# Kernel tuning notes

Measured on AMD Instinct MI355X. Metric: run time of the kernel, lower is better.

The kernel has to match this reference:

```python
import jax, jax.numpy as jnp
import numpy as np

ALPHA = 0.2  # LeakyReLU negative slope


def setup_inputs() -> dict:
    key = jax.random.key(0)
    k1, k2 = jax.random.split(key)
    B, N, Fin, Fout = 4, 4096, 256, 128
    h = jax.random.normal(k1, (B, N, Fin), dtype=jnp.float32)
    adj = jnp.zeros((B, N, N), dtype=bool)  # unused by the original forward
    # Linear(in,out,bias=False); stored as [in,out] for h @ W
    W = jax.random.normal(k2, (Fin, Fout), dtype=jnp.float32) * (1.0 / np.sqrt(Fin))
    return {"h": h, "adj": adj, "W": W}


def reference(h, adj, W):
    # h: [B,N,Fin], W: [Fin,Fout]
    hp = jnp.einsum("bnf,fo->bno", h, W)                    # [B,N,Fout]
    e = jnp.einsum("bnd,bmd->bnm", hp, hp)                  # [B,N,N]
    e = jnp.where(e >= 0, e, ALPHA * e)                      # LeakyReLU
    attn = jax.nn.softmax(e, axis=1)                         # softmax over dim=1 (rows)
    # torch: sum_j( hp[b,i] * attn[b,i,j] ) == hp[b,i] * sum_j attn[b,i,j]
    row_mass = jnp.sum(attn, axis=2, keepdims=True)          # [B,N,1]
    return hp * row_mass
```

## Files before the change

kernel.cpp:

```cpp
#include <hip/hip_runtime.h>
#include <hip/hip_bf16.h>

#define ALPHA 0.2f

constexpr int BN   = 4;
constexpr int NN   = 4096;
constexpr int FIN  = 256;
constexpr int FOUT = 128;
constexpr int NT   = 64;
constexpr int NPAIR = NT * (NT + 1) / 2;

typedef __attribute__((ext_vector_type(8))) short bf16x8;
typedef __attribute__((ext_vector_type(4))) float f32x4;

#define MFMA16(a, b, c) __builtin_amdgcn_mfma_f32_16x16x32_bf16((a), (b), (c), 0, 0, 0)

template<int CTRL>
__device__ __forceinline__ float dpp_mov(float x) {
    return __int_as_float(__builtin_amdgcn_update_dpp(
        __float_as_int(x), __float_as_int(x), CTRL, 0xF, 0xF, false));
}
__device__ __forceinline__ float rsum16(float x) {
    x += dpp_mov<0x128>(x);
    x += dpp_mov<0x124>(x);
    x += dpp_mov<0x122>(x);
    x += dpp_mov<0x121>(x);
    return x;
}
__device__ __forceinline__ float rmax16(float x) {
    x = fmaxf(x, dpp_mov<0x128>(x));
    x = fmaxf(x, dpp_mov<0x124>(x));
    x = fmaxf(x, dpp_mov<0x122>(x));
    x = fmaxf(x, dpp_mov<0x121>(x));
    return x;
}

__device__ __forceinline__ void split8(const float* x, uint4& H, uint4& L) {
    ushort hb[8], lb[8];
    #pragma unroll
    for (int i = 0; i < 8; ++i) {
        float xv = x[i];
        __hip_bfloat16 hh = __float2bfloat16(xv);
        float hf = __bfloat162float(hh);
        __hip_bfloat16 lw = __float2bfloat16(xv - hf);
        hb[i] = reinterpret_cast<const ushort&>(hh);
        lb[i] = reinterpret_cast<const ushort&>(lw);
    }
    H = make_uint4((uint)hb[0] | ((uint)hb[1] << 16), (uint)hb[2] | ((uint)hb[3] << 16),
                   (uint)hb[4] | ((uint)hb[5] << 16), (uint)hb[6] | ((uint)hb[7] << 16));
    L = make_uint4((uint)lb[0] | ((uint)lb[1] << 16), (uint)lb[2] | ((uint)lb[3] << 16),
                   (uint)lb[4] | ((uint)lb[5] << 16), (uint)lb[6] | ((uint)lb[7] << 16));
}

template<int ROWS, int KGSH>
__device__ __forceinline__ void stage_split(const float* __restrict__ src, int strideF,
                                            ushort* hi, ushort* lo, int tid) {
    constexpr int KG = 1 << KGSH;
    #pragma unroll
    for (int idx = tid; idx < ROWS * KG; idx += 256) {
        int row = idx >> KGSH, g = idx & (KG - 1);
        const float4* p4 = reinterpret_cast<const float4*>(src + (size_t)row * strideF + g * 8);
        float4 u = p4[0], v = p4[1];
        float x[8] = {u.x, u.y, u.z, u.w, v.x, v.y, v.z, v.w};
        uint4 H, L;
        split8(x, H, L);
        int gran = (row << KGSH) + (g ^ (row & 7));
        reinterpret_cast<uint4*>(hi)[gran] = H;
        reinterpret_cast<uint4*>(lo)[gran] = L;
    }
}
template<int ROWS, int KGSH>
__device__ __forceinline__ void stage_copy(const ushort* __restrict__ src, int strideU,
                                           ushort* dst, int tid) {
    constexpr int KG = 1 << KGSH;
    #pragma unroll
    for (int idx = tid; idx < ROWS * KG; idx += 256) {
        int row = idx >> KGSH, g = idx & (KG - 1);
        uint4 vv = *reinterpret_cast<const uint4*>(src + (size_t)row * strideU + g * 8);
        reinterpret_cast<uint4*>(dst)[(row << KGSH) + (g ^ (row & 7))] = vv;
    }
}
__device__ __forceinline__ bf16x8 frag16(const ushort* s, int rowbase, int kstep, int kgsh, int lane) {
    int r = rowbase + (lane & 15);
    int g = kstep * 4 + (lane >> 4);
    int gran = (r << kgsh) + (g ^ (r & 7));
    return *reinterpret_cast<const bf16x8*>(s + gran * 8);
}

__global__ void k_prepW(const float* __restrict__ W, ushort* __restrict__ Wt_hi,
                        ushort* __restrict__ Wt_lo) {
    int idx = blockIdx.x * 256 + threadIdx.x;
    if (idx >= FOUT * (FIN / 8)) return;
    int n = idx >> 5, g = idx & 31;
    float x[8];
    #pragma unroll
    for (int i = 0; i < 8; ++i) x[i] = W[(size_t)(g * 8 + i) * FOUT + n];
    uint4 H, L;
    split8(x, H, L);
    reinterpret_cast<uint4*>(Wt_hi)[n * 32 + g] = H;
    reinterpret_cast<uint4*>(Wt_lo)[n * 32 + g] = L;
}

__global__ __launch_bounds__(256)
void k_hp(const float* __restrict__ h, const ushort* __restrict__ Wt_hi,
          const ushort* __restrict__ Wt_lo, float* __restrict__ hp) {
    __shared__ __align__(16) ushort Ah[64 * 64], Al[64 * 64];
    __shared__ __align__(16) ushort Bh[128 * 64], Bl[128 * 64];
    const int tid = threadIdx.x, lane = tid & 63, wid = tid >> 6;
    const int wy = wid >> 1, wx = wid & 1;
    const int ibase = blockIdx.x * 64;
    f32x4 z = {0.f, 0.f, 0.f, 0.f};
    f32x4 acc[2][4] = {{z, z, z, z}, {z, z, z, z}};
    for (int kt = 0; kt < 4; ++kt) {
        __syncthreads();
        stage_split<64, 3>(h + (size_t)ibase * FIN + kt * 64, FIN, Ah, Al, tid);
        stage_copy<128, 3>(Wt_hi + kt * 64, FIN, Bh, tid);
        stage_copy<128, 3>(Wt_lo + kt * 64, FIN, Bl, tid);
        __syncthreads();
        #pragma unroll
        for (int pr = 0; pr < 3; ++pr) {
            const ushort* A = (pr == 2) ? Al : Ah;
            const ushort* B = (pr == 1) ? Bl : Bh;
            #pragma unroll
            for (int ks = 0; ks < 2; ++ks) {
                bf16x8 a0 = frag16(A, wy * 32, ks, 3, lane);
                bf16x8 a1 = frag16(A, wy * 32 + 16, ks, 3, lane);
                #pragma unroll
                for (int c = 0; c < 4; ++c) {
                    bf16x8 bb = frag16(B, wx * 64 + c * 16, ks, 3, lane);
                    acc[0][c] = MFMA16(a0, bb, acc[0][c]);
                    acc[1][c] = MFMA16(a1, bb, acc[1][c]);
                }
            }
        }
    }
    #pragma unroll
    for (int r = 0; r < 2; ++r)
        #pragma unroll
        for (int c = 0; c < 4; ++c)
            #pragma unroll
            for (int p = 0; p < 4; ++p) {
                int row = ibase + wy * 32 + r * 16 + (lane >> 4) * 4 + p;
                int col = wx * 64 + c * 16 + (lane & 15);
                hp[(size_t)row * FOUT + col] = acc[r][c][p];
            }
}

__global__ void k_fragpack(const float* __restrict__ hp, ushort* __restrict__ hi,
                           ushort* __restrict__ lo) {
    int t = blockIdx.x * 256 + threadIdx.x;
    int l = t & 63, ks = (t >> 6) & 3, P = (t >> 8) & 255, b = t >> 16;
    int row = P * 16 + (l & 15), c8 = ks * 4 + (l >> 4);
    const float* src = hp + ((size_t)b * NN + row) * FOUT + c8 * 8;
    const float4* p4 = reinterpret_cast<const float4*>(src);
    float4 u = p4[0], v = p4[1];
    float x[8] = {u.x, u.y, u.z, u.w, v.x, v.y, v.z, v.w};
    uint4 H, L;
    split8(x, H, L);
    size_t o = (((size_t)b * 256 + P) * 4 + ks) * 64 + l;
    reinterpret_cast<uint4*>(hi)[o] = H;
    reinterpret_cast<uint4*>(lo)[o] = L;
}

__device__ __forceinline__ void decode2(int bid, int wid, int& b, int& ti, int& tj) {
    int slot = bid & 7;
    b = slot >> 1;
    int sub = ((bid >> 3) << 1) | (slot & 1);
    int tb = sub * 4 + wid;
    int t = 0, width = NT;
    while (tb >= width) { tb -= width; --width; ++t; }
    ti = t;
    tj = t + tb;
}

__device__ __forceinline__ void etile_fl(const uint4* __restrict__ H4,
                                         const uint4* __restrict__ L4,
                                         int pi, int pj, int lane, f32x4 acc[4][4]) {
    #pragma unroll
    for (int ks = 0; ks < 4; ++ks) {
        bf16x8 aH[4], aL[4];
        #pragma unroll
        for (int r = 0; r < 4; ++r) {
            size_t idx = ((size_t)(pi + r) * 4 + ks) * 64 + lane;
            aH[r] = *reinterpret_cast<const bf16x8*>(&H4[idx]);
            aL[r] = *reinterpret_cast<const bf16x8*>(&L4[idx]);
        }
        #pragma unroll
        for (int c = 0; c < 4; ++c) {
            size_t jdx = ((size_t)(pj + c) * 4 + ks) * 64 + lane;
            bf16x8 bH = *reinterpret_cast<const bf16x8*>(&H4[jdx]);
            bf16x8 bL = *reinterpret_cast<const bf16x8*>(&L4[jdx]);
            #pragma unroll
            for (int r = 0; r < 4; ++r) {
                acc[r][c] = MFMA16(aH[r], bH, acc[r][c]);
                acc[r][c] = MFMA16(aH[r], bL, acc[r][c]);
                acc[r][c] = MFMA16(aL[r], bH, acc[r][c]);
            }
        }
    }
}

__global__ __launch_bounds__(256, 3)
void k_stats(const ushort* __restrict__ hp_hi, const ushort* __restrict__ hp_lo,
             float* __restrict__ m_part, float* __restrict__ s_part) {
    const int tid = threadIdx.x, lane = tid & 63, wid = tid >> 6;
    const int lrow = lane & 15, lg = lane >> 4;
    int b, ti, tj;
    decode2(blockIdx.x, wid, b, ti, tj);
    const uint4* H4 = reinterpret_cast<const uint4*>(hp_hi) + (size_t)b * 256 * 256;
    const uint4* L4 = reinterpret_cast<const uint4*>(hp_lo) + (size_t)b * 256 * 256;
    const int ibase = ti * 64, jbase = tj * 64;
    f32x4 z = {0.f, 0.f, 0.f, 0.f};
    f32x4 acc[4][4] = {{z,z,z,z},{z,z,z,z},{z,z,z,z},{z,z,z,z}};
    etile_fl(H4, L4, ti * 4, tj * 4, lane, acc);
    #pragma unroll
    for (int r = 0; r < 4; ++r)
        #pragma unroll
        for (int c = 0; c < 4; ++c)
            #pragma unroll
            for (int p = 0; p < 4; ++p) {
                float x = acc[r][c][p];
                acc[r][c][p] = fmaxf(x, ALPHA * x);
            }
    {
        float* mp = m_part + (size_t)(b * NT + tj) * NN;
        float* sp = s_part + (size_t)(b * NT + tj) * NN;
        #pragma unroll
        for (int r = 0; r < 4; ++r)
            #pragma unroll
            for (int p = 0; p < 4; ++p) {
                float mx = fmaxf(fmaxf(acc[r][0][p], acc[r][1][p]),
                                 fmaxf(acc[r][2][p], acc[r][3][p]));
                mx = rmax16(mx);
                float se = 0.f;
                #pragma unroll
                for (int c = 0; c < 4; ++c) se += __expf(acc[r][c][p] - mx);
                se = rsum16(se);
                if (lrow == 0) {
                    int i = ibase + r * 16 + lg * 4 + p;
                    mp[i] = mx;
                    sp[i] = se;
                }
            }
    }
    if (ti != tj) {
        float* mp = m_part + (size_t)(b * NT + ti) * NN;
        float* sp = s_part + (size_t)(b * NT + ti) * NN;
        #pragma unroll
        for (int c = 0; c < 4; ++c) {
            float mx = -1e30f;
            #pragma unroll
            for (int r = 0; r < 4; ++r)
                #pragma unroll
                for (int p = 0; p < 4; ++p) mx = fmaxf(mx, acc[r][c][p]);
            mx = fmaxf(mx, __shfl_xor(mx, 16));
            mx = fmaxf(mx, __shfl_xor(mx, 32));
            float se = 0.f;
            #pragma unroll
            for (int r = 0; r < 4; ++r)
                #pragma unroll
                for (int p = 0; p < 4; ++p) se += __expf(acc[r][c][p] - mx);
            se += __shfl_xor(se, 16);
            se += __shfl_xor(se, 32);
            if (lane < 16) {
                int j = jbase + c * 16 + lane;
                mp[j] = mx;
                sp[j] = se;
            }
        }
    }
}

__global__ void k_merge(const float* __restrict__ m_part, const float* __restrict__ s_part,
                        float* __restrict__ m_fin, float* __restrict__ inv_s) {
    int idx = blockIdx.x * 256 + threadIdx.x;
    if (idx >= BN * NN) return;
    int b = idx >> 12, row = idx & (NN - 1);
    const float* mp = m_part + (size_t)b * NT * NN + row;
    const float* sp = s_part + (size_t)b * NT * NN + row;
    float M = -1e30f;
    for (int k = 0; k < NT; ++k) M = fmaxf(M, mp[(size_t)k * NN]);
    float S = 0.f;
    for (int k = 0; k < NT; ++k) S += sp[(size_t)k * NN] * __expf(mp[(size_t)k * NN] - M);
    m_fin[idx] = M;
    inv_s[idx] = 1.f / S;
}

__global__ __launch_bounds__(256, 3)
void k_mass(const ushort* __restrict__ hp_hi, const ushort* __restrict__ hp_lo,
            const float* __restrict__ m_fin, const float* __restrict__ inv_s,
            float* __restrict__ rs_part) {
    const int tid = threadIdx.x, lane = tid & 63, wid = tid >> 6;
    const int lrow = lane & 15, lg = lane >> 4;
    int b, ti, tj;
    decode2(blockIdx.x, wid, b, ti, tj);
    const uint4* H4 = reinterpret_cast<const uint4*>(hp_hi) + (size_t)b * 256 * 256;
    const uint4* L4 = reinterpret_cast<const uint4*>(hp_lo) + (size_t)b * 256 * 256;
    const int ibase = ti * 64, jbase = tj * 64;
    f32x4 z = {0.f, 0.f, 0.f, 0.f};
    f32x4 acc[4][4] = {{z,z,z,z},{z,z,z,z},{z,z,z,z},{z,z,z,z}};
    etile_fl(H4, L4, ti * 4, tj * 4, lane, acc);
    const float* mf = m_fin + (size_t)b * NN;
    const float* isv = inv_s + (size_t)b * NN;
    float mj[4], sj[4];
    #pragma unroll
    for (int c = 0; c < 4; ++c) {
        int j = jbase + c * 16 + lrow;
        mj[c] = mf[j];
        sj[c] = isv[j];
    }
    {
        float* rs = rs_part + (size_t)(b * NT + tj) * NN;
        #pragma unroll
        for (int r = 0; r < 4; ++r)
            #pragma unroll
            for (int p = 0; p < 4; ++p) {
                float s = 0.f;
                #pragma unroll
                for (int c = 0; c < 4; ++c) {
                    float x = acc[r][c][p];
                    float g = fmaxf(x, ALPHA * x);
                    s += __expf(g - mj[c]) * sj[c];
                }
                s = rsum16(s);
                if (lrow == 0) rs[ibase + r * 16 + lg * 4 + p] = s;
            }
    }
    if (ti != tj) {
        float mi[4][4], si_[4][4];
        #pragma unroll
        for (int r = 0; r < 4; ++r)
            #pragma unroll
            for (int p = 0; p < 4; ++p) {
                int i = ibase + r * 16 + lg * 4 + p;
                mi[r][p] = mf[i];
                si_[r][p] = isv[i];
            }
        float* rs = rs_part + (size_t)(b * NT + ti) * NN;
        #pragma unroll
        for (int c = 0; c < 4; ++c) {
            float s2 = 0.f;
            #pragma unroll
            for (int r = 0; r < 4; ++r)
                #pragma unroll
                for (int p = 0; p < 4; ++p) {
                    float x = acc[r][c][p];
                    float g = fmaxf(x, ALPHA * x);
                    s2 += __expf(g - mi[r][p]) * si_[r][p];
                }
            s2 += __shfl_xor(s2, 16);
            s2 += __shfl_xor(s2, 32);
            if (lane < 16) rs[jbase + c * 16 + lane] = s2;
        }
    }
}

__global__ void k_scale(const float* __restrict__ rs_part, float* __restrict__ out) {
    int idx = blockIdx.x * 256 + threadIdx.x;
    if (idx >= BN * NN * FOUT / 4) return;
    int row = idx >> 5;
    int b = row >> 12, i = row & (NN - 1);
    const float* rs = rs_part + (size_t)b * NT * NN + i;
    float rm = 0.f;
    for (int k = 0; k < NT; ++k) rm += rs[(size_t)k * NN];
    float4 v = reinterpret_cast<float4*>(out)[idx];
    v.x *= rm; v.y *= rm; v.z *= rm; v.w *= rm;
    reinterpret_cast<float4*>(out)[idx] = v;
}

extern "C" void kernel_launch(void* const* d_in, const int* in_sizes, int n_in,
                              void* d_out, int out_size, void* d_ws, size_t ws_size,
                              hipStream_t stream) {
    (void)in_sizes; (void)n_in; (void)out_size; (void)ws_size;
    const float* h = (const float*)d_in[0];
    const float* W = (const float*)d_in[2];
    float* out = (float*)d_out;
    ushort* hp_hi = (ushort*)d_ws;
    ushort* hp_lo = hp_hi + (size_t)BN * NN * FOUT;
    ushort* Wt_hi = hp_lo + (size_t)BN * NN * FOUT;
    ushort* Wt_lo = Wt_hi + FOUT * FIN;
    float* m_part = (float*)(Wt_lo + FOUT * FIN);
    float* s_part = m_part + (size_t)BN * NT * NN;
    float* m_fin  = s_part + (size_t)BN * NT * NN;
    float* inv_s  = m_fin + (size_t)BN * NN;
    float* rs_part = inv_s + (size_t)BN * NN;

    k_prepW<<<(FOUT * (FIN / 8) + 255) / 256, 256, 0, stream>>>(W, Wt_hi, Wt_lo);
    k_hp<<<BN * NN / 64, 256, 0, stream>>>(h, Wt_hi, Wt_lo, out);
    k_fragpack<<<BN * 256 * 4 * 64 / 256, 256, 0, stream>>>(out, hp_hi, hp_lo);
    k_stats<<<BN * NPAIR / 4, 256, 0, stream>>>(hp_hi, hp_lo, m_part, s_part);
    k_merge<<<(BN * NN + 255) / 256, 256, 0, stream>>>(m_part, s_part, m_fin, inv_s);
    k_mass<<<BN * NPAIR / 4, 256, 0, stream>>>(hp_hi, hp_lo, m_fin, inv_s, rs_part);
    k_scale<<<(BN * NN * FOUT / 4 + 255) / 256, 256, 0, stream>>>(rs_part, out);
}
```

Baseline: 418.6 us.

## Switch Gram tiles to 32x32x16 MFMA with repacked fragment layout

Replaces the 16x16x32 bf16 MFMA tiling of each 64x64 Gram tile with a 2x2 grid of 32x32x16 MFMAs, and repacks the hi/lo bf16 fragments in k_fragpack to match the 32-row operand layout. Row and column reductions in k_stats and k_mass are rewritten for the new accumulator lane mapping. Wave priority is raised around the MFMA loop. The goal is fewer operand loads per FLOP and higher MFMA throughput, at the cost of different reduction shuffles and per-element m/s loads in the column pass of k_mass.

```diff
diff --git a/kernel.cpp b/kernel.cpp
--- a/kernel.cpp
+++ b/kernel.cpp
@@ -12,8 +12,10 @@
 
 typedef __attribute__((ext_vector_type(8))) short bf16x8;
 typedef __attribute__((ext_vector_type(4))) float f32x4;
+typedef __attribute__((ext_vector_type(16))) float f32x16;
 
 #define MFMA16(a, b, c) __builtin_amdgcn_mfma_f32_16x16x32_bf16((a), (b), (c), 0, 0, 0)
+#define MFMA32(a, b, c) __builtin_amdgcn_mfma_f32_32x32x16_bf16((a), (b), (c), 0, 0, 0)
 
 template<int CTRL>
 __device__ __forceinline__ float dpp_mov(float x) {
@@ -149,17 +151,16 @@
 __global__ void k_fragpack(const float* __restrict__ hp, ushort* __restrict__ hi,
                            ushort* __restrict__ lo) {
     int t = blockIdx.x * 256 + threadIdx.x;
-    int l = t & 63, ks = (t >> 6) & 3, P = (t >> 8) & 255, b = t >> 16;
-    int row = P * 16 + (l & 15), c8 = ks * 4 + (l >> 4);
+    int l = t & 63, s = (t >> 6) & 7, Q = (t >> 9) & 127, b = t >> 16;
+    int row = Q * 32 + (l & 31), c8 = s * 2 + (l >> 5);
     const float* src = hp + ((size_t)b * NN + row) * FOUT + c8 * 8;
     const float4* p4 = reinterpret_cast<const float4*>(src);
     float4 u = p4[0], v = p4[1];
     float x[8] = {u.x, u.y, u.z, u.w, v.x, v.y, v.z, v.w};
     uint4 H, L;
     split8(x, H, L);
-    size_t o = (((size_t)b * 256 + P) * 4 + ks) * 64 + l;
-    reinterpret_cast<uint4*>(hi)[o] = H;
-    reinterpret_cast<uint4*>(lo)[o] = L;
+    reinterpret_cast<uint4*>(hi)[t] = H;
+    reinterpret_cast<uint4*>(lo)[t] = L;
 }
 
 __device__ __forceinline__ void decode2(int bid, int wid, int& b, int& ti, int& tj) {
@@ -173,71 +174,78 @@
     tj = t + tb;
 }
 
-__device__ __forceinline__ void etile_fl(const uint4* __restrict__ H4,
-                                         const uint4* __restrict__ L4,
-                                         int pi, int pj, int lane, f32x4 acc[4][4]) {
-    #pragma unroll
-    for (int ks = 0; ks < 4; ++ks) {
-        bf16x8 aH[4], aL[4];
-        #pragma unroll
-        for (int r = 0; r < 4; ++r) {
-            size_t idx = ((size_t)(pi + r) * 4 + ks) * 64 + lane;
-            aH[r] = *reinterpret_cast<const bf16x8*>(&H4[idx]);
-            aL[r] = *reinterpret_cast<const bf16x8*>(&L4[idx]);
-        }
-        #pragma unroll
-        for (int c = 0; c < 4; ++c) {
-            size_t jdx = ((size_t)(pj + c) * 4 + ks) * 64 + lane;
-            bf16x8 bH = *reinterpret_cast<const bf16x8*>(&H4[jdx]);
-            bf16x8 bL = *reinterpret_cast<const bf16x8*>(&L4[jdx]);
-            #pragma unroll
-            for (int r = 0; r < 4; ++r) {
-                acc[r][c] = MFMA16(aH[r], bH, acc[r][c]);
-                acc[r][c] = MFMA16(aH[r], bL, acc[r][c]);
-                acc[r][c] = MFMA16(aL[r], bH, acc[r][c]);
-            }
-        }
-    }
+__device__ __forceinline__ void etile32(const uint4* __restrict__ H4,
+                                        const uint4* __restrict__ L4,
+                                        int ti, int tj, int lane, f32x16 acc[2][2]) {
+    __builtin_amdgcn_s_setprio(1);
+    #pragma unroll
+    for (int s = 0; s < 8; ++s) {
+        bf16x8 aH[2], aL[2], bH[2], bL[2];
+        #pragma unroll
+        for (int R = 0; R < 2; ++R) {
+            size_t idx = ((size_t)((ti * 2 + R) * 8 + s)) * 64 + lane;
+            aH[R] = *reinterpret_cast<const bf16x8*>(&H4[idx]);
+            aL[R] = *reinterpret_cast<const bf16x8*>(&L4[idx]);
+        }
+        #pragma unroll
+        for (int C = 0; C < 2; ++C) {
+            size_t jdx = ((size_t)((tj * 2 + C) * 8 + s)) * 64 + lane;
+            bH[C] = *reinterpret_cast<const bf16x8*>(&H4[jdx]);
+            bL[C] = *reinterpret_cast<const bf16x8*>(&L4[jdx]);
+        }
+        #pragma unroll
+        for (int R = 0; R < 2; ++R)
+            #pragma unroll
+            for (int C = 0; C < 2; ++C) {
+                acc[R][C] = MFMA32(aH[R], bH[C], acc[R][C]);
+                acc[R][C] = MFMA32(aH[R], bL[C], acc[R][C]);
+                acc[R][C] = MFMA32(aL[R], bH[C], acc[R][C]);
+            }
+    }
+    __builtin_amdgcn_s_setprio(0);
 }
 
 __global__ __launch_bounds__(256, 3)
 void k_stats(const ushort* __restrict__ hp_hi, const ushort* __restrict__ hp_lo,
              float* __restrict__ m_part, float* __restrict__ s_part) {
     const int tid = threadIdx.x, lane = tid & 63, wid = tid >> 6;
-    const int lrow = lane & 15, lg = lane >> 4;
     int b, ti, tj;
     decode2(blockIdx.x, wid, b, ti, tj);
-    const uint4* H4 = reinterpret_cast<const uint4*>(hp_hi) + (size_t)b * 256 * 256;
-    const uint4* L4 = reinterpret_cast<const uint4*>(hp_lo) + (size_t)b * 256 * 256;
+    const uint4* H4 = reinterpret_cast<const uint4*>(hp_hi) + (size_t)b * 65536;
+    const uint4* L4 = reinterpret_cast<const uint4*>(hp_lo) + (size_t)b * 65536;
     const int ibase = ti * 64, jbase = tj * 64;
-    f32x4 z = {0.f, 0.f, 0.f, 0.f};
-    f32x4 acc[4][4] = {{z,z,z,z},{z,z,z,z},{z,z,z,z},{z,z,z,z}};
-    etile_fl(H4, L4, ti * 4, tj * 4, lane, acc);
-    #pragma unroll
-    for (int r = 0; r < 4; ++r)
-        #pragma unroll
-        for (int c = 0; c < 4; ++c)
-            #pragma unroll
-            for (int p = 0; p < 4; ++p) {
-                float x = acc[r][c][p];
-                acc[r][c][p] = fmaxf(x, ALPHA * x);
+    f32x16 acc[2][2];
+    #pragma unroll
+    for (int R = 0; R < 2; ++R)
+        #pragma unroll
+        for (int C = 0; C < 2; ++C)
+            #pragma unroll
+            for (int q = 0; q < 16; ++q) acc[R][C][q] = 0.f;
+    etile32(H4, L4, ti, tj, lane, acc);
+    #pragma unroll
+    for (int R = 0; R < 2; ++R)
+        #pragma unroll
+        for (int C = 0; C < 2; ++C)
+            #pragma unroll
+            for (int q = 0; q < 16; ++q) {
+                float x = acc[R][C][q];
+                acc[R][C][q] = fmaxf(x, ALPHA * x);
             }
     {
         float* mp = m_part + (size_t)(b * NT + tj) * NN;
         float* sp = s_part + (size_t)(b * NT + tj) * NN;
         #pragma unroll
-        for (int r = 0; r < 4; ++r)
-            #pragma unroll
-            for (int p = 0; p < 4; ++p) {
-                float mx = fmaxf(fmaxf(acc[r][0][p], acc[r][1][p]),
-                                 fmaxf(acc[r][2][p], acc[r][3][p]));
+        for (int R = 0; R < 2; ++R)
+            #pragma unroll
+            for (int q = 0; q < 16; ++q) {
+                float mx = fmaxf(acc[R][0][q], acc[R][1][q]);
                 mx = rmax16(mx);
-                float se = 0.f;
-                #pragma unroll
-                for (int c = 0; c < 4; ++c) se += __expf(acc[r][c][p] - mx);
+                mx = fmaxf(mx, __shfl_xor(mx, 16));
+                float se = __expf(acc[R][0][q] - mx) + __expf(acc[R][1][q] - mx);
                 se = rsum16(se);
-                if (lrow == 0) {
-                    int i = ibase + r * 16 + lg * 4 + p;
+                se += __shfl_xor(se, 16);
+                if ((lane & 31) == 0) {
+                    int i = ibase + R * 32 + (q & 3) + 8 * (q >> 2) + 4 * (lane >> 5);
                     mp[i] = mx;
                     sp[i] = se;
                 }
@@ -247,23 +255,21 @@
         float* mp = m_part + (size_t)(b * NT + ti) * NN;
         float* sp = s_part + (size_t)(b * NT + ti) * NN;
         #pragma unroll
-        for (int c = 0; c < 4; ++c) {
+        for (int C = 0; C < 2; ++C) {
             float mx = -1e30f;
             #pragma unroll
-            for (int r = 0; r < 4; ++r)
+            for (int R = 0; R < 2; ++R)
                 #pragma unroll
-                for (int p = 0; p < 4; ++p) mx = fmaxf(mx, acc[r][c][p]);
-            mx = fmaxf(mx, __shfl_xor(mx, 16));
+                for (int q = 0; q < 16; ++q) mx = fmaxf(mx, acc[R][C][q]);
             mx = fmaxf(mx, __shfl_xor(mx, 32));
             float se = 0.f;
             #pragma unroll
-            for (int r = 0; r < 4; ++r)
+            for (int R = 0; R < 2; ++R)
                 #pragma unroll
-                for (int p = 0; p < 4; ++p) se += __expf(acc[r][c][p] - mx);
-            se += __shfl_xor(se, 16);
+                for (int q = 0; q < 16; ++q) se += __expf(acc[R][C][q] - mx);
             se += __shfl_xor(se, 32);
-            if (lane < 16) {
-                int j = jbase + c * 16 + lane;
+            if (lane < 32) {
+                int j = jbase + C * 32 + lane;
                 mp[j] = mx;
                 sp[j] = se;
             }
@@ -291,66 +297,62 @@
             const float* __restrict__ m_fin, const float* __restrict__ inv_s,
             float* __restrict__ rs_part) {
     const int tid = threadIdx.x, lane = tid & 63, wid = tid >> 6;
-    const int lrow = lane & 15, lg = lane >> 4;
     int b, ti, tj;
     decode2(blockIdx.x, wid, b, ti, tj);
-    const uint4* H4 = reinterpret_cast<const uint4*>(hp_hi) + (size_t)b * 256 * 256;
-    const uint4* L4 = reinterpret_cast<const uint4*>(hp_lo) + (size_t)b * 256 * 256;
+    const uint4* H4 = reinterpret_cast<const uint4*>(hp_hi) + (size_t)b * 65536;
+    const uint4* L4 = reinterpret_cast<const uint4*>(hp_lo) + (size_t)b * 65536;
     const int ibase = ti * 64, jbase = tj * 64;
-    f32x4 z = {0.f, 0.f, 0.f, 0.f};
-    f32x4 acc[4][4] = {{z,z,z,z},{z,z,z,z},{z,z,z,z},{z,z,z,z}};
-    etile_fl(H4, L4, ti * 4, tj * 4, lane, acc);
+    f32x16 acc[2][2];
+    #pragma unroll
+    for (int R = 0; R < 2; ++R)
+        #pragma unroll
+        for (int C = 0; C < 2; ++C)
+            #pragma unroll
+            for (int q = 0; q < 16; ++q) acc[R][C][q] = 0.f;
+    etile32(H4, L4, ti, tj, lane, acc);
     const float* mf = m_fin + (size_t)b * NN;
     const float* isv = inv_s + (size_t)b * NN;
-    float mj[4], sj[4];
-    #pragma unroll
-    for (int c = 0; c < 4; ++c) {
-        int j = jbase + c * 16 + lrow;
-        mj[c] = mf[j];
-        sj[c] = isv[j];
+    float mj[2], sj[2];
+    #pragma unroll
+    for (int C = 0; C < 2; ++C) {
+        int j = jbase + C * 32 + (lane & 31);
+        mj[C] = mf[j];
+        sj[C] = isv[j];
     }
     {
         float* rs = rs_part + (size_t)(b * NT + tj) * NN;
         #pragma unroll
-        for (int r = 0; r < 4; ++r)
-            #pragma unroll
-            for (int p = 0; p < 4; ++p) {
-                float s = 0.f;
-                #pragma unroll
-                for (int c = 0; c < 4; ++c) {
-                    float x = acc[r][c][p];
-                    float g = fmaxf(x, ALPHA * x);
-                    s += __expf(g - mj[c]) * sj[c];
-                }
+        for (int R = 0; R < 2; ++R)
+            #pragma unroll
+            for (int q = 0; q < 16; ++q) {
+                float x0 = acc[R][0][q], x1 = acc[R][1][q];
+                float g0 = fmaxf(x0, ALPHA * x0), g1 = fmaxf(x1, ALPHA * x1);
+                float s = __expf(g0 - mj[0]) * sj[0] + __expf(g1 - mj[1]) * sj[1];
                 s = rsum16(s);
-                if (lrow == 0) rs[ibase + r * 16 + lg * 4 + p] = s;
+                s += __shfl_xor(s, 16);
+                if ((lane & 31) == 0)
+                    rs[ibase + R * 32 + (q & 3) + 8 * (q >> 2) + 4 * (lane >> 5)] = s;
             }
     }
     if (ti != tj) {
-        float mi[4][4], si_[4][4];
-        #pragma unroll
-        for (int r = 0; r < 4; ++r)
-            #pragma unroll
-            for (int p = 0; p < 4; ++p) {
-                int i = ibase + r * 16 + lg * 4 + p;
-                mi[r][p] = mf[i];
-                si_[r][p] = isv[i];
+        float s2[2] = {0.f, 0.f};
+        #pragma unroll
+        for (int R = 0; R < 2; ++R)
+            #pragma unroll
+            for (int q = 0; q < 16; ++q) {
+                int i = ibase + R * 32 + (q & 3) + 8 * (q >> 2) + 4 * (lane >> 5);
+                float m_i = mf[i];
+                float s_i = isv[i];
+                float x0 = acc[R][0][q], x1 = acc[R][1][q];
+                float g0 = fmaxf(x0, ALPHA * x0), g1 = fmaxf(x1, ALPHA * x1);
+                s2[0] += __expf(g0 - m_i) * s_i;
+                s2[1] += __expf(g1 - m_i) * s_i;
             }
         float* rs = rs_part + (size_t)(b * NT + ti) * NN;
         #pragma unroll
-        for (int c = 0; c < 4; ++c) {
-            float s2 = 0.f;
-            #pragma unroll
-            for (int r = 0; r < 4; ++r)
-                #pragma unroll
-                for (int p = 0; p < 4; ++p) {
-                    float x = acc[r][c][p];
-                    float g = fmaxf(x, ALPHA * x);
-                    s2 += __expf(g - mi[r][p]) * si_[r][p];
-                }
-            s2 += __shfl_xor(s2, 16);
-            s2 += __shfl_xor(s2, 32);
-            if (lane < 16) rs[jbase + c * 16 + lane] = s2;
+        for (int C = 0; C < 2; ++C) {
+            float v = s2[C] + __shfl_xor(s2[C], 32);
+            if (lane < 32) rs[jbase + C * 32 + lane] = v;
         }
     }
 }
@@ -387,7 +389,7 @@
 
     k_prepW<<<(FOUT * (FIN / 8) + 255) / 256, 256, 0, stream>>>(W, Wt_hi, Wt_lo);
     k_hp<<<BN * NN / 64, 256, 0, stream>>>(h, Wt_hi, Wt_lo, out);
-    k_fragpack<<<BN * 256 * 4 * 64 / 256, 256, 0, stream>>>(out, hp_hi, hp_lo);
+    k_fragpack<<<BN * 128 * 8 * 64 / 256, 256, 0, stream>>>(out, hp_hi, hp_lo);
     k_stats<<<BN * NPAIR / 4, 256, 0, stream>>>(hp_hi, hp_lo, m_part, s_part);
     k_merge<<<(BN * NN + 255) / 256, 256, 0, stream>>>(m_part, s_part, m_fin, inv_s);
     k_mass<<<BN * NPAIR / 4, 256, 0, stream>>>(hp_hi, hp_lo, m_fin, inv_s, rs_part);
```

Result: slower. 444.2 us (+6.1%).
